# Kernel optimization log

Hardware: AMD Instinct MI355X
Metric: run time of the kernel (lower is better)

Reference implementation:

```python
import jax, jax.numpy as jnp
import numpy as np

N = 1_000_000
Km = 16
Ks = 64
LB, RT = -1.0, 1.0  # hemi=False -> lb=(-1,-1), rt=(1,1)
TWO_PI = 2.0 * np.pi


def setup_inputs() -> dict:
    key = jax.random.key(0)
    ks = jax.random.split(key, 12)
    r = jax.random.uniform(ks[0], (N, 1), jnp.float32, -0.999, 0.999)
    z = jax.random.uniform(ks[1], (N, 1), jnp.float32, 0.0, TWO_PI)
    theta_w = jax.random.normal(ks[2], (1, Ks), jnp.float32)
    theta_h = jax.random.normal(ks[3], (1, Ks), jnp.float32)
    theta_d = jax.random.normal(ks[4], (1, Ks - 1), jnp.float32)
    W1 = jax.random.normal(ks[5], (1, 64), jnp.float32)
    b1 = jax.random.normal(ks[6], (64,), jnp.float32) * 0.1
    W2 = jax.random.normal(ks[7], (64, 64), jnp.float32) / np.float32(np.sqrt(64))
    b2 = jax.random.normal(ks[8], (64,), jnp.float32) * 0.1
    W3 = jax.random.normal(ks[9], (64, 3 * Km), jnp.float32) / np.float32(np.sqrt(64))
    b3 = jax.random.normal(ks[10], (3 * Km,), jnp.float32) * 0.1
    return dict(r=r, z=z, theta_w=theta_w, theta_h=theta_h, theta_d=theta_d,
                W1=W1, b1=b1, W2=W2, b2=b2, W3=W3, b3=b3)


def _spline(r, theta_w, theta_h, theta_d):
    # Unconditional rational-quadratic circular spline on (LB, RT).
    width = jax.nn.softmax(theta_w, axis=1) * (RT - LB)    # [1,Ks]
    height = jax.nn.softmax(theta_h, axis=1) * (RT - LB)
    zero = jnp.zeros((1, 1), width.dtype)
    x_ks = jnp.concatenate([zero, jnp.cumsum(width, axis=1)], axis=1) + LB   # [1,Ks+1]
    y_ks = jnp.concatenate([zero, jnp.cumsum(height, axis=1)], axis=1) + LB
    bnd = jnp.full((1, 1), (RT - LB) / (RT - LB), width.dtype)
    derivs = jnp.concatenate([bnd, jax.nn.softplus(theta_d) + 0.001, bnd], axis=1)  # [1,Ks+1]

    x = r[:, 0]                                             # [N]
    k = jnp.searchsorted(x_ks[0], x)                        # left side, matches torch default
    k = jnp.where(k == 0, 1, k)
    k = jnp.where(k == Ks + 1, Ks, k)
    k = k - 1
    nk = k + 1
    x_k, x_nk = x_ks[0, k], x_ks[0, nk]
    y_k, y_nk = y_ks[0, k], y_ks[0, nk]
    d_k, d_nk = derivs[0, k], derivs[0, nk]

    s_k = (y_nk - y_k) / (x_nk - x_k)
    eps = (x - x_k) / (x_nk - x_k)
    denom = s_k + (d_nk + d_k - 2.0 * s_k) * eps * (1.0 - eps)
    tx = y_k + (y_nk - y_k) * (s_k * eps ** 2 + d_k * eps * (1.0 - eps)) / denom
    dtx = s_k ** 2 * (d_nk * eps ** 2 + 2.0 * s_k * eps * (1.0 - eps) + d_k * (1.0 - eps) ** 2) / denom ** 2
    return tx[:, None], dtx


def _mobius(x, r, W1, b1, W2, b2, W3, b3):
    # Conditional Mobius transform on the circle; conditioner = 2-hidden MLP on r.
    h = jax.nn.relu(r @ W1 + b1)
    h = jax.nn.relu(h @ W2 + b2)
    theta = h @ W3 + b3                                     # [N,3Km]
    weights = jax.nn.softmax(theta[:, :Km], axis=1)         # [N,Km]
    w = theta[:, Km:].reshape(-1, Km, 2)                    # [N,Km,2]
    w = 0.99 / (1.0 + jnp.linalg.norm(w, axis=-1, keepdims=True)) * w

    def h_map(zv, w):
        # zv: [M,2] broadcast against w: [N,Km,2]
        diff = zv[:, None, :] - w
        wn2 = jnp.sum(w * w, axis=-1, keepdims=True)
        dn2 = jnp.sum(diff * diff, axis=-1, keepdims=True)
        return (1.0 - wn2) / dn2 * diff - w

    zv = jnp.concatenate([jnp.cos(x), jnp.sin(x)], axis=1)  # [N,2]
    h_z = h_map(zv, w)                                      # [N,Km,2]
    h_0 = h_map(jnp.array([[1.0, 0.0]], zv.dtype), w)
    radians = jnp.arctan2(h_z[..., 1], h_z[..., 0])
    shifts = jnp.arctan2(h_0[..., 1], h_0[..., 0])
    tx = radians - shifts
    tx = jnp.where(tx >= 0, tx, tx + TWO_PI)
    t = jnp.sum(weights * tx, axis=1, keepdims=True)        # [N,1]

    # Jacobian magnitude: dh/dz is c*(I - 2 u u^T) (scaled reflection), applied to dz/dtheta
    diff = zv[:, None, :] - w
    dn = jnp.linalg.norm(diff, axis=-1)                     # [N,Km]
    u = diff / dn[..., None]
    dz = jnp.concatenate([-jnp.sin(x), jnp.cos(x)], axis=1) # [N,2]
    c = (1.0 - jnp.sum(w * w, axis=-1)) / dn ** 2           # [N,Km]
    udz = jnp.sum(u * dz[:, None, :], axis=-1)              # [N,Km]
    dh = c[..., None] * (dz[:, None, :] - 2.0 * u * udz[..., None])  # [N,Km,2]
    dt = jnp.sum(jnp.linalg.norm(dh, axis=-1) * weights, axis=1)     # [N]
    return t, dt


def reference(r, z, theta_w, theta_h, theta_d, W1, b1, W2, b2, W3, b3):
    tr, dtr = _spline(r, theta_w, theta_h, theta_d)
    tz, dtz = _mobius(z, r, W1, b1, W2, b2, W3, b3)
    ldj = jnp.log(dtr) + jnp.log(dtz)
    return tr, tz, ldj
```

## Files before the change

### kernel.cpp

```cpp
#include <hip/hip_runtime.h>
#include <math.h>

#define KM 16
#define KS 64
#define TWO_PI_F 6.283185307179586477f

#define WS_SXK   0
#define WS_SYK   65
#define WS_SDK   130
#define WS_KNOT  195
#define WS_A     259
#define WS_B     (259 + 4225)
#define WS_SROOT 8709
#define WS_COEF  12872
#define WS_NEED  (12872 + 4225 * 96)

__device__ __forceinline__ float frcp(float x) { return __builtin_amdgcn_rcpf(x); }

__device__ __forceinline__ float fast_atan2(float y, float x) {
    const float ax = fabsf(x), ay = fabsf(y);
    const float mx = fmaxf(ax, ay), mn = fminf(ax, ay);
    const float t = mn * frcp(mx);
    const float s = t * t;
    float p = -0.01172120f;
    p = fmaf(p, s,  0.05265332f);
    p = fmaf(p, s, -0.11643287f);
    p = fmaf(p, s,  0.19354346f);
    p = fmaf(p, s, -0.33262347f);
    p = fmaf(p, s,  0.99997726f);
    p = p * t;
    p = (ay > ax) ? (1.57079632679f - p) : p;
    p = (x < 0.0f) ? (3.14159265359f - p) : p;
    p = (y < 0.0f) ? -p : p;
    return p;
}

__global__ __launch_bounds__(256)
void precompute_full(const float* __restrict__ theta_w,
                     const float* __restrict__ theta_h,
                     const float* __restrict__ theta_d,
                     const float* __restrict__ W1,
                     const float* __restrict__ b1,
                     const float* __restrict__ W2,
                     const float* __restrict__ b2,
                     const float* __restrict__ W3,
                     const float* __restrict__ b3,
                     float* __restrict__ ws)
{
    __shared__ float sW1[64], sb1[64], tjs[64], sknotS[64];
    __shared__ int   srnk[64];
    __shared__ float sW2[64 * 64];
    __shared__ float sW3[64 * 48];
    __shared__ float sb3[48];
    __shared__ float sAv[64], sBv[64], rroot[64], rsort[64], rmid[65];

    const int tid = threadIdx.x;
    const int v = blockIdx.x;

    if (tid < 64) { sW1[tid] = W1[tid]; sb1[tid] = b1[tid]; }
    {
        const float4* __restrict__ a = (const float4*)W2;
        float4* b = (float4*)sW2;
        for (int t = tid; t < 1024; t += 256) b[t] = a[t];
    }
    {
        const float4* __restrict__ a = (const float4*)W3;
        float4* b = (float4*)sW3;
        for (int t = tid; t < 768; t += 256) b[t] = a[t];
    }
    if (tid < 48) sb3[tid] = b3[tid];
    __syncthreads();

    if (tid < 64)
        tjs[tid] = (sW1[tid] != 0.0f) ? (-sb1[tid] / sW1[tid]) : INFINITY;
    __syncthreads();
    if (tid < 64) {
        const float t = tjs[tid];
        int rk = 0;
        #pragma unroll 1
        for (int k2 = 0; k2 < 64; k2++) {
            const float tk = tjs[k2];
            rk += (tk < t || (tk == t && k2 < tid)) ? 1 : 0;
        }
        srnk[tid] = rk;
        sknotS[rk] = t;
    }
    __syncthreads();

    if (tid < 64) {
        const int i = tid;
        float cA = 0.0f, cB = b2[i];
        #pragma unroll 1
        for (int j = 0; j < 64; j++) {
            const float w1 = sW1[j];
            const float bb = sb1[j];
            const float w2 = sW2[j * 64 + i];
            if (w1 > 0.0f) {
                if (srnk[j] < v)  { cA = fmaf(w1, w2, cA); cB = fmaf(bb, w2, cB); }
            } else if (w1 < 0.0f) {
                if (srnk[j] >= v) { cA = fmaf(w1, w2, cA); cB = fmaf(bb, w2, cB); }
            } else {
                cB = fmaf(fmaxf(bb, 0.0f), w2, cB);
            }
        }
        sAv[i] = cA; sBv[i] = cB;
    }
    __syncthreads();

    if (tid < 64)
        rroot[tid] = (sAv[tid] != 0.0f) ? (-sBv[tid] / sAv[tid]) : INFINITY;
    __syncthreads();
    if (tid < 64) {
        const float t = rroot[tid];
        int rk = 0;
        #pragma unroll 1
        for (int k2 = 0; k2 < 64; k2++) {
            const float tk = rroot[k2];
            rk += (tk < t || (tk == t && k2 < tid)) ? 1 : 0;
        }
        rsort[rk] = t;
        ws[WS_SROOT + v * 64 + rk] = t;
    }
    __syncthreads();

    const float x_lo = (v == 0)  ? -1.0f : sknotS[v - 1];
    const float x_hi = (v == 64) ?  1.0f : sknotS[v];
    if (tid < 65) {
        const int s = tid;
        const float lo = (s == 0)  ? x_lo : fmaxf(x_lo, rsort[s - 1]);
        const float hi = (s == 64) ? x_hi : fminf(x_hi, rsort[s]);
        rmid[s] = 0.5f * (lo + hi);
    }
    __syncthreads();

    for (int p = tid; p < 65 * 48; p += 256) {
        const int s = p / 48;
        const int o = p - 48 * s;
        const float rm = rmid[s];
        float a = 0.0f, b = sb3[o];
        #pragma unroll 4
        for (int j = 0; j < 64; j++) {
            const float A = sAv[j], B = sBv[j];
            const float w3 = sW3[j * 48 + o];
            const float m = (fmaf(A, rm, B) > 0.0f) ? w3 : 0.0f;
            a = fmaf(A, m, a);
            b = fmaf(B, m, b);
        }
        float* __restrict__ row = ws + WS_COEF + (v * 65 + s) * 96;
        row[2 * o]     = a;
        row[2 * o + 1] = b;
    }

    if (v == 0 && tid < 64) {
        ws[WS_KNOT + tid] = sknotS[tid];

        float vw = theta_w[tid];
        float vh = theta_h[tid];
        float mw = vw, mh = vh;
        #pragma unroll
        for (int off = 32; off > 0; off >>= 1) {
            mw = fmaxf(mw, __shfl_xor(mw, off));
            mh = fmaxf(mh, __shfl_xor(mh, off));
        }
        const float ew = expf(vw - mw);
        const float eh = expf(vh - mh);
        float sumw = ew, sumh = eh;
        #pragma unroll
        for (int off = 32; off > 0; off >>= 1) {
            sumw += __shfl_xor(sumw, off);
            sumh += __shfl_xor(sumh, off);
        }
        float cw = ew / sumw * 2.0f;
        float ch = eh / sumh * 2.0f;
        #pragma unroll
        for (int off = 1; off < 64; off <<= 1) {
            const float uw = __shfl_up(cw, off);
            const float uh = __shfl_up(ch, off);
            if (tid >= off) { cw += uw; ch += uh; }
        }
        ws[WS_SXK + 1 + tid] = cw - 1.0f;
        ws[WS_SYK + 1 + tid] = ch - 1.0f;
        if (tid < KS - 1) {
            const float x = theta_d[tid];
            const float sp = (x > 20.0f) ? x : log1pf(expf(x));
            ws[WS_SDK + 1 + tid] = sp + 0.001f;
        }
        if (tid == 0) {
            ws[WS_SXK] = -1.0f;
            ws[WS_SYK] = -1.0f;
            ws[WS_SDK] = 1.0f;
            ws[WS_SDK + KS] = 1.0f;
        }
    }
}

__global__ __launch_bounds__(256)
void mobius_spline_kernel(const float* __restrict__ r_in,
                          const float* __restrict__ z_in,
                          const float* __restrict__ ws,
                          float* __restrict__ out,
                          int n)
{
    __shared__ float sxk[KS + 1], syk[KS + 1], sdk[KS + 1];
    __shared__ float sknot[KS];
    __shared__ float sroots[65 * 65];

    const int tid = threadIdx.x;

    for (int t2 = tid; t2 < 65; t2 += 256) {
        sxk[t2] = ws[WS_SXK + t2];
        syk[t2] = ws[WS_SYK + t2];
        sdk[t2] = ws[WS_SDK + t2];
    }
    for (int t2 = tid; t2 < 64; t2 += 256) sknot[t2] = ws[WS_KNOT + t2];
    for (int t2 = tid; t2 < 65 * 64; t2 += 256) {
        const int v2 = t2 >> 6, m = t2 & 63;
        sroots[v2 * 65 + m] = ws[WS_SROOT + t2];
    }
    __syncthreads();

    const int idx = blockIdx.x * 256 + tid;
    if (idx >= n) return;

    const float rv = r_in[idx];
    const float zz = z_in[idx];

    int lo = 0, hi = KS + 1;
    while (lo < hi) {
        const int mid = (lo + hi) >> 1;
        if (sxk[mid] < rv) lo = mid + 1; else hi = mid;
    }
    int k = lo;
    k = (k == 0) ? 1 : k;
    k = (k == KS + 1) ? KS : k;
    k -= 1;
    const float x_k = sxk[k], x_nk = sxk[k + 1];
    const float y_k = syk[k], y_nk = syk[k + 1];
    const float d_k = sdk[k], d_nk = sdk[k + 1];
    const float rdx = frcp(x_nk - x_k);
    const float dy  = y_nk - y_k;
    const float s_k = dy * rdx;
    const float eps = (rv - x_k) * rdx;
    const float ome = 1.0f - eps;
    const float den = s_k + (d_nk + d_k - 2.0f * s_k) * eps * ome;
    const float rden = frcp(den);
    const float tr  = fmaf(dy * (s_k * eps * eps + d_k * eps * ome), rden, y_k);
    const float dtr = s_k * s_k * (d_nk * eps * eps + 2.0f * s_k * eps * ome + d_k * ome * ome)
                      * rden * rden;

    int lo2 = 0, hi2 = KS;
    while (lo2 < hi2) {
        const int mid = (lo2 + hi2) >> 1;
        if (sknot[mid] < rv) lo2 = mid + 1; else hi2 = mid;
    }
    const int v = lo2;
    const int rbase = v * 65;
    int lo3 = 0, hi3 = 64;
    while (lo3 < hi3) {
        const int mid = (lo3 + hi3) >> 1;
        if (sroots[rbase + mid] < rv) lo3 = mid + 1; else hi3 = mid;
    }
    const int s = lo3;

    const float4* __restrict__ row4 =
        (const float4*)(ws + WS_COEF + (size_t)(v * 65 + s) * 96);

    float th[16];
    #pragma unroll
    for (int o8 = 0; o8 < 8; o8++) {
        const float4 c = row4[o8];
        th[2 * o8]     = fmaf(c.x, rv, c.y);
        th[2 * o8 + 1] = fmaf(c.z, rv, c.w);
    }
    float mx = th[0];
    #pragma unroll
    for (int q = 1; q < 16; q++) mx = fmaxf(mx, th[q]);

    float cz, sz;
    __sincosf(zz, &sz, &cz);

    float wsum = 0.0f, tsum = 0.0f, dsum = 0.0f;

    #pragma unroll 4
    for (int q = 0; q < 16; q++) {
        const float4 c = row4[8 + q];
        const float rwx = fmaf(c.x, rv, c.y);
        const float rwy = fmaf(c.z, rv, c.w);
        const float nrm = __builtin_amdgcn_sqrtf(rwx * rwx + rwy * rwy);
        const float scl = 0.99f * frcp(1.0f + nrm);
        const float wxx = scl * rwx, wyy = scl * rwy;
        const float wn2 = wxx * wxx + wyy * wyy;
        const float omw = 1.0f - wn2;
        const float dzx = cz - wxx, dzy = sz - wyy;
        const float dn2z = dzx * dzx + dzy * dzy;
        const float cf = omw * frcp(dn2z);
        const float hzx = cf * dzx - wxx;
        const float hzy = cf * dzy - wyy;
        const float d0x = 1.0f - wxx, d0y = -wyy;
        const float dn20 = d0x * d0x + d0y * d0y;
        const float c0 = omw * frcp(dn20);
        const float h0x = c0 * d0x - wxx;
        const float h0y = c0 * d0y - wyy;
        const float cross = hzy * h0x - hzx * h0y;
        const float dotp  = hzx * h0x + hzy * h0y;
        float tx = fast_atan2(cross, dotp);
        tx = (tx >= 0.0f) ? tx : tx + TWO_PI_F;

        const float ew = __expf(th[q] - mx);
        wsum += ew;
        tsum += ew * tx;
        dsum += ew * cf;
    }

    const float inv = frcp(wsum);
    const float tz  = tsum * inv;
    const float dtz = dsum * inv;
    const float ldj = __logf(dtr) + __logf(dtz);

    out[idx]         = tr;
    out[n + idx]     = tz;
    out[2 * n + idx] = ldj;
}

__global__ __launch_bounds__(256)
void precompute_fb(const float* __restrict__ theta_w,
                   const float* __restrict__ theta_h,
                   const float* __restrict__ theta_d,
                   const float* __restrict__ W1,
                   const float* __restrict__ b1,
                   const float* __restrict__ W2,
                   const float* __restrict__ b2,
                   float* __restrict__ ws)
{
    __shared__ float sW1[64], sb1[64], tjs[64];
    __shared__ int   srnk[64];
    __shared__ float sW2[64 * 64];

    const int tid = threadIdx.x;

    if (tid < 64) {
        const float w1 = W1[tid];
        const float bb = b1[tid];
        sW1[tid] = w1;
        sb1[tid] = bb;
        tjs[tid] = (w1 != 0.0f) ? (-bb / w1) : INFINITY;
    }
    {
        const float4* __restrict__ W2v = (const float4*)W2;
        float4* __restrict__ sW2v = (float4*)sW2;
        for (int t2 = tid; t2 < 1024; t2 += 256) sW2v[t2] = W2v[t2];
    }
    __syncthreads();

    if (tid < 64) {
        const float t = tjs[tid];
        int rk = 0;
        #pragma unroll 1
        for (int k2 = 0; k2 < 64; k2++) {
            const float tk = tjs[k2];
            rk += (tk < t || (tk == t && k2 < tid)) ? 1 : 0;
        }
        srnk[tid] = rk;
    }
    __syncthreads();

    if (blockIdx.x == 0 && tid < 64) {
        ws[WS_KNOT + srnk[tid]] = tjs[tid];
        float vw = theta_w[tid];
        float vh = theta_h[tid];
        float mw = vw, mh = vh;
        #pragma unroll
        for (int off = 32; off > 0; off >>= 1) {
            mw = fmaxf(mw, __shfl_xor(mw, off));
            mh = fmaxf(mh, __shfl_xor(mh, off));
        }
        const float ew = expf(vw - mw);
        const float eh = expf(vh - mh);
        float sumw = ew, sumh = eh;
        #pragma unroll
        for (int off = 32; off > 0; off >>= 1) {
            sumw += __shfl_xor(sumw, off);
            sumh += __shfl_xor(sumh, off);
        }
        float cw = ew / sumw * 2.0f;
        float ch = eh / sumh * 2.0f;
        #pragma unroll
        for (int off = 1; off < 64; off <<= 1) {
            const float uw = __shfl_up(cw, off);
            const float uh = __shfl_up(ch, off);
            if (tid >= off) { cw += uw; ch += uh; }
        }
        ws[WS_SXK + 1 + tid] = cw - 1.0f;
        ws[WS_SYK + 1 + tid] = ch - 1.0f;
        if (tid < KS - 1) {
            const float x = theta_d[tid];
            const float sp = (x > 20.0f) ? x : log1pf(expf(x));
            ws[WS_SDK + 1 + tid] = sp + 0.001f;
        }
        if (tid == 0) {
            ws[WS_SXK] = -1.0f;
            ws[WS_SYK] = -1.0f;
            ws[WS_SDK] = 1.0f;
            ws[WS_SDK + KS] = 1.0f;
        }
    }

    const int p = blockIdx.x * 256 + tid;
    if (p < 65 * 64) {
        const int v = p >> 6;
        const int i = p & 63;
        float cA = 0.0f;
        float cB = b2[i];
        #pragma unroll 1
        for (int j = 0; j < 64; j++) {
            const float w1 = sW1[j];
            const float bb = sb1[j];
            const float w2 = sW2[j * 64 + i];
            if (w1 > 0.0f) {
                if (srnk[j] < v)  { cA = fmaf(w1, w2, cA); cB = fmaf(bb, w2, cB); }
            } else if (w1 < 0.0f) {
                if (srnk[j] >= v) { cA = fmaf(w1, w2, cA); cB = fmaf(bb, w2, cB); }
            } else {
                cB = fmaf(fmaxf(bb, 0.0f), w2, cB);
            }
        }
        ws[WS_A + v * 65 + i] = cA;
        ws[WS_B + v * 65 + i] = cB;
    }
}

__global__ __launch_bounds__(256)
void mobius_spline_fb(const float* __restrict__ r_in,
                      const float* __restrict__ z_in,
                      const float* __restrict__ W3,
                      const float* __restrict__ b3,
                      const float* __restrict__ ws,
                      float* __restrict__ out,
                      int n)
{
    __shared__ float sxk[KS + 1], syk[KS + 1], sdk[KS + 1];
    __shared__ float sknot[KS];
    __shared__ float sA[65 * 65], sB[65 * 65];

    const int tid = threadIdx.x;

    for (int t2 = tid; t2 < 65; t2 += 256) {
        sxk[t2] = ws[WS_SXK + t2];
        syk[t2] = ws[WS_SYK + t2];
        sdk[t2] = ws[WS_SDK + t2];
    }
    for (int t2 = tid; t2 < 64; t2 += 256) sknot[t2] = ws[WS_KNOT + t2];
    for (int t2 = tid; t2 < 4225; t2 += 256) {
        sA[t2] = ws[WS_A + t2];
        sB[t2] = ws[WS_B + t2];
    }
    __syncthreads();

    const int idx = blockIdx.x * 256 + tid;
    if (idx >= n) return;

    const float rv = r_in[idx];
    const float zz = z_in[idx];

    int lo = 0, hi = KS + 1;
    while (lo < hi) {
        const int mid = (lo + hi) >> 1;
        if (sxk[mid] < rv) lo = mid + 1; else hi = mid;
    }
    int k = lo;
    k = (k == 0) ? 1 : k;
    k = (k == KS + 1) ? KS : k;
    k -= 1;
    const float x_k = sxk[k], x_nk = sxk[k + 1];
    const float y_k = syk[k], y_nk = syk[k + 1];
    const float d_k = sdk[k], d_nk = sdk[k + 1];
    const float rdx = frcp(x_nk - x_k);
    const float dy  = y_nk - y_k;
    const float s_k = dy * rdx;
    const float eps = (rv - x_k) * rdx;
    const float ome = 1.0f - eps;
    const float den = s_k + (d_nk + d_k - 2.0f * s_k) * eps * ome;
    const float rden = frcp(den);
    const float tr  = fmaf(dy * (s_k * eps * eps + d_k * eps * ome), rden, y_k);
    const float dtr = s_k * s_k * (d_nk * eps * eps + 2.0f * s_k * eps * ome + d_k * ome * ome)
                      * rden * rden;

    int lo2 = 0, hi2 = KS;
    while (lo2 < hi2) {
        const int mid = (lo2 + hi2) >> 1;
        if (sknot[mid] < rv) lo2 = mid + 1; else hi2 = mid;
    }
    const int abase = lo2 * 65;

    float th[16], wx[16], wy[16];
    #pragma unroll
    for (int q = 0; q < 16; q++) {
        th[q] = b3[q];
        wx[q] = b3[16 + 2 * q];
        wy[q] = b3[17 + 2 * q];
    }

    #pragma unroll 4
    for (int i = 0; i < 64; i++) {
        const float hv = fmaxf(fmaf(rv, sA[abase + i], sB[abase + i]), 0.0f);
        const float* __restrict__ w3r = &W3[i * 48];
        #pragma unroll
        for (int q = 0; q < 16; q++) {
            th[q] = fmaf(hv, w3r[q],          th[q]);
            wx[q] = fmaf(hv, w3r[16 + 2 * q], wx[q]);
            wy[q] = fmaf(hv, w3r[17 + 2 * q], wy[q]);
        }
    }

    float mx = th[0];
    #pragma unroll
    for (int q = 1; q < 16; q++) mx = fmaxf(mx, th[q]);

    float cz, sz;
    __sincosf(zz, &sz, &cz);

    float wsum = 0.0f, tsum = 0.0f, dsum = 0.0f;

    #pragma unroll
    for (int q = 0; q < 16; q++) {
        const float rwx = wx[q], rwy = wy[q];
        const float nrm = __builtin_amdgcn_sqrtf(rwx * rwx + rwy * rwy);
        const float scl = 0.99f * frcp(1.0f + nrm);
        const float wxx = scl * rwx, wyy = scl * rwy;
        const float wn2 = wxx * wxx + wyy * wyy;
        const float omw = 1.0f - wn2;
        const float dzx = cz - wxx, dzy = sz - wyy;
        const float dn2z = dzx * dzx + dzy * dzy;
        const float cf = omw * frcp(dn2z);
        const float hzx = cf * dzx - wxx;
        const float hzy = cf * dzy - wyy;
        const float d0x = 1.0f - wxx, d0y = -wyy;
        const float dn20 = d0x * d0x + d0y * d0y;
        const float c0 = omw * frcp(dn20);
        const float h0x = c0 * d0x - wxx;
        const float h0y = c0 * d0y - wyy;
        const float cross = hzy * h0x - hzx * h0y;
        const float dotp  = hzx * h0x + hzy * h0y;
        float tx = fast_atan2(cross, dotp);
        tx = (tx >= 0.0f) ? tx : tx + TWO_PI_F;

        const float ew = __expf(th[q] - mx);
        wsum += ew;
        tsum += ew * tx;
        dsum += ew * cf;
    }

    const float inv = frcp(wsum);
    const float tz  = tsum * inv;
    const float dtz = dsum * inv;
    const float ldj = __logf(dtr) + __logf(dtz);

    out[idx]         = tr;
    out[n + idx]     = tz;
    out[2 * n + idx] = ldj;
}

extern "C" void kernel_launch(void* const* d_in, const int* in_sizes, int n_in,
                              void* d_out, int out_size, void* d_ws, size_t ws_size,
                              hipStream_t stream) {
    const int n = in_sizes[0];
    float* ws = (float*)d_ws;
    const int blocks = (n + 255) / 256;

    if (ws_size >= (size_t)WS_NEED * sizeof(float)) {
        hipLaunchKernelGGL(precompute_full, dim3(65), dim3(256), 0, stream,
                           (const float*)d_in[2], (const float*)d_in[3],
                           (const float*)d_in[4], (const float*)d_in[5],
                           (const float*)d_in[6], (const float*)d_in[7],
                           (const float*)d_in[8], (const float*)d_in[9],
                           (const float*)d_in[10], ws);
        hipLaunchKernelGGL(mobius_spline_kernel, dim3(blocks), dim3(256), 0, stream,
                           (const float*)d_in[0], (const float*)d_in[1],
                           (const float*)ws, (float*)d_out, n);
    } else {
        hipLaunchKernelGGL(precompute_fb, dim3(17), dim3(256), 0, stream,
                           (const float*)d_in[2], (const float*)d_in[3],
                           (const float*)d_in[4], (const float*)d_in[5],
                           (const float*)d_in[6], (const float*)d_in[7],
                           (const float*)d_in[8], ws);
        hipLaunchKernelGGL(mobius_spline_fb, dim3(blocks), dim3(256), 0, stream,
                           (const float*)d_in[0], (const float*)d_in[1],
                           (const float*)d_in[9], (const float*)d_in[10],
                           (const float*)ws, (float*)d_out, n);
    }
}
```

Before: 167.4 us.

## Build per-segment layer-3 coefficients by incremental prefix sums over sorted roots

```diff
diff --git a/kernel.cpp b/kernel.cpp
--- a/kernel.cpp
+++ b/kernel.cpp
@@ -52,7 +52,8 @@
     __shared__ float sW2[64 * 64];
     __shared__ float sW3[64 * 48];
     __shared__ float sb3[48];
-    __shared__ float sAv[64], sBv[64], rroot[64], rsort[64], rmid[65];
+    __shared__ float sAv[64], sBv[64], rroot[64];
+    __shared__ int   jinv[64];
 
     const int tid = threadIdx.x;
     const int v = blockIdx.x;
@@ -77,7 +78,7 @@
     if (tid < 64) {
         const float t = tjs[tid];
         int rk = 0;
-        #pragma unroll 1
+        #pragma unroll 8
         for (int k2 = 0; k2 < 64; k2++) {
             const float tk = tjs[k2];
             rk += (tk < t || (tk == t && k2 < tid)) ? 1 : 0;
@@ -90,7 +91,7 @@
     if (tid < 64) {
         const int i = tid;
         float cA = 0.0f, cB = b2[i];
-        #pragma unroll 1
+        #pragma unroll 8
         for (int j = 0; j < 64; j++) {
             const float w1 = sW1[j];
             const float bb = sb1[j];
@@ -113,42 +114,42 @@
     if (tid < 64) {
         const float t = rroot[tid];
         int rk = 0;
-        #pragma unroll 1
+        #pragma unroll 8
         for (int k2 = 0; k2 < 64; k2++) {
             const float tk = rroot[k2];
             rk += (tk < t || (tk == t && k2 < tid)) ? 1 : 0;
         }
-        rsort[rk] = t;
+        jinv[rk] = tid;
         ws[WS_SROOT + v * 64 + rk] = t;
     }
     __syncthreads();
 
-    const float x_lo = (v == 0)  ? -1.0f : sknotS[v - 1];
-    const float x_hi = (v == 64) ?  1.0f : sknotS[v];
-    if (tid < 65) {
-        const int s = tid;
-        const float lo = (s == 0)  ? x_lo : fmaxf(x_lo, rsort[s - 1]);
-        const float hi = (s == 64) ? x_hi : fminf(x_hi, rsort[s]);
-        rmid[s] = 0.5f * (lo + hi);
-    }
-    __syncthreads();
-
-    for (int p = tid; p < 65 * 48; p += 256) {
-        const int s = p / 48;
-        const int o = p - 48 * s;
-        const float rm = rmid[s];
+    if (tid < 48) {
+        const int o = tid;
         float a = 0.0f, b = sb3[o];
-        #pragma unroll 4
+        #pragma unroll 8
         for (int j = 0; j < 64; j++) {
             const float A = sAv[j], B = sBv[j];
             const float w3 = sW3[j * 48 + o];
-            const float m = (fmaf(A, rm, B) > 0.0f) ? w3 : 0.0f;
+            const bool act = (A < 0.0f) || (A == 0.0f && B > 0.0f);
+            const float m = act ? w3 : 0.0f;
             a = fmaf(A, m, a);
             b = fmaf(B, m, b);
         }
-        float* __restrict__ row = ws + WS_COEF + (v * 65 + s) * 96;
-        row[2 * o]     = a;
-        row[2 * o + 1] = b;
+        float* __restrict__ rowbase = ws + WS_COEF + (size_t)(v * 65) * 96;
+        rowbase[2 * o]     = a;
+        rowbase[2 * o + 1] = b;
+        #pragma unroll 4
+        for (int s = 1; s <= 64; s++) {
+            const int js = jinv[s - 1];
+            const float A = sAv[js], B = sBv[js];
+            const float w3 = sW3[js * 48 + o];
+            const float sgn = (A > 0.0f) ? w3 : ((A < 0.0f) ? -w3 : 0.0f);
+            a = fmaf(A, sgn, a);
+            b = fmaf(B, sgn, b);
+            rowbase[s * 96 + 2 * o]     = a;
+            rowbase[s * 96 + 2 * o + 1] = b;
+        }
     }
 
     if (v == 0 && tid < 64) {
@@ -281,7 +282,7 @@
 
     float wsum = 0.0f, tsum = 0.0f, dsum = 0.0f;
 
-    #pragma unroll 4
+    #pragma unroll
     for (int q = 0; q < 16; q++) {
         const float4 c = row4[8 + q];
         const float rwx = fmaf(c.x, rv, c.y);
@@ -355,7 +356,7 @@
     if (tid < 64) {
         const float t = tjs[tid];
         int rk = 0;
-        #pragma unroll 1
+        #pragma unroll 8
         for (int k2 = 0; k2 < 64; k2++) {
             const float tk = tjs[k2];
             rk += (tk < t || (tk == t && k2 < tid)) ? 1 : 0;
```

New measurement: 152.5 us. 1.1x faster.
